# Optimization experiments

Hardware: AMD Instinct MI355X
Metric: run time of the kernel (lower is better)

## Reference

```python
import jax, jax.numpy as jnp
import numpy as np

B = 8
WS = 7; NH = 8; HD = 16; C = 128; HP = 56; SHIFT = 3; L = HP * HP
SCALE = HD ** -0.5


def _rel_pos_index():
    coords = np.stack(np.meshgrid(np.arange(WS), np.arange(WS), indexing='ij')).reshape(2, -1)
    rel = (coords[:, :, None] - coords[:, None, :]).transpose(1, 2, 0)
    rel[:, :, 0] += WS - 1
    rel[:, :, 1] += WS - 1
    rel[:, :, 0] *= 2 * WS - 1
    return rel.sum(-1)  # (49, 49) int


def _attn_mask():
    img = np.zeros((HP, HP))
    cnt = 0
    for h in (slice(0, -WS), slice(-WS, -SHIFT), slice(-SHIFT, None)):
        for w in (slice(0, -WS), slice(-WS, -SHIFT), slice(-SHIFT, None)):
            img[h, w] = cnt
            cnt += 1
    m = img.reshape(HP // WS, WS, HP // WS, WS).transpose(0, 2, 1, 3).reshape(-1, WS * WS)
    am = m[:, None, :] - m[:, :, None]
    return np.where(am != 0, -100.0, 0.0).astype(np.float32)  # (64, 49, 49)


REL_IDX = _rel_pos_index()
ATTN_MASK = jnp.asarray(_attn_mask())


def _ln(x, g, b):
    mu = x.mean(-1, keepdims=True)
    v = ((x - mu) ** 2).mean(-1, keepdims=True)
    return (x - mu) / jnp.sqrt(v + 1e-5) * g + b


def setup_inputs() -> dict:
    key = jax.random.key(0)
    ks = iter(jax.random.split(key, 40))
    n = lambda shape: jax.random.normal(next(ks), shape, dtype=jnp.float32) * 0.02
    z = lambda shape: jnp.zeros(shape, dtype=jnp.float32)
    o = lambda shape: jnp.ones(shape, dtype=jnp.float32)
    return dict(
        infrared=jax.random.normal(next(ks), (B, 1, 224, 224), dtype=jnp.float32),
        visible=jax.random.normal(next(ks), (B, 1, 224, 224), dtype=jnp.float32),
        patch_w=n((16, C)), patch_b=z((C,)),
        pn_g=o((C,)), pn_b=z((C,)),
        pos_embed=n((1, L, C)),
        norm1_g=o((2, C)), norm1_b=z((2, C)),
        qkv_w=n((2, C, 3 * C)), qkv_b=z((2, 3 * C)),
        proj_w=n((2, C, C)), proj_b=z((2, C)),
        norm2_g=o((2, C)), norm2_b=z((2, C)),
        fc1_w=n((2, C, 4 * C)), fc1_b=z((2, 4 * C)),
        fc2_w=n((2, 4 * C, C)), fc2_b=z((2, C)),
        rpb=n((2, (2 * WS - 1) ** 2, NH)),
        normf_g=o((C,)), normf_b=z((C,)),
        head1_w=n((C, 256)), head1_b=z((256,)),
        head2_w=n((256, 1)), head2_b=z((1,)),
    )


def reference(infrared, visible, patch_w, patch_b, pn_g, pn_b, pos_embed,
              norm1_g, norm1_b, qkv_w, qkv_b, proj_w, proj_b,
              norm2_g, norm2_b, fc1_w, fc1_b, fc2_w, fc2_b, rpb,
              normf_g, normf_b, head1_w, head1_b, head2_w, head2_b):
    Bv = visible.shape[0]
    # 4x4 stride-4 conv on 1-channel input == patchify + matmul
    x = visible.reshape(Bv, HP, 4, HP, 4).transpose(0, 1, 3, 2, 4).reshape(Bv, L, 16)
    x = _ln(x @ patch_w + patch_b, pn_g, pn_b) + pos_embed  # (B, 3136, 128)

    def win_attn(xw, i, mask):
        Bn, N = xw.shape[0], WS * WS
        qkv = (xw @ qkv_w[i] + qkv_b[i]).reshape(Bn, N, 3, NH, HD).transpose(2, 0, 3, 1, 4)
        q, k, v = qkv[0], qkv[1], qkv[2]
        attn = jnp.einsum('bhnd,bhmd->bhnm', q * SCALE, k)  # (Bn, H, 49, 49)
        bias = rpb[i][REL_IDX.reshape(-1)].reshape(N, N, NH).transpose(2, 0, 1)
        attn = attn + bias[None]
        if mask is not None:
            attn = attn.reshape(Bv, -1, NH, N, N) + mask[None, :, None]
            attn = attn.reshape(Bn, NH, N, N)
        attn = jax.nn.softmax(attn, axis=-1)
        out = jnp.einsum('bhnm,bhmd->bhnd', attn, v).transpose(0, 2, 1, 3).reshape(Bn, N, C)
        return out @ proj_w[i] + proj_b[i]

    def block(x, i, shift):
        shortcut = x
        h = _ln(x, norm1_g[i], norm1_b[i]).reshape(Bv, HP, HP, C)
        if shift:
            h = jnp.roll(h, (-SHIFT, -SHIFT), (1, 2))
        w = h.reshape(Bv, 8, WS, 8, WS, C).transpose(0, 1, 3, 2, 4, 5).reshape(-1, WS * WS, C)
        w = win_attn(w, i, ATTN_MASK if shift else None)
        h = w.reshape(Bv, 8, 8, WS, WS, C).transpose(0, 1, 3, 2, 4, 5).reshape(Bv, HP, HP, C)
        if shift:
            h = jnp.roll(h, (SHIFT, SHIFT), (1, 2))
        x = shortcut + h.reshape(Bv, L, C)  # drop_path is identity at inference
        m = _ln(x, norm2_g[i], norm2_b[i])
        m = jax.nn.gelu(m @ fc1_w[i] + fc1_b[i]) @ fc2_w[i] + fc2_b[i]
        return x + m

    x = block(x, 0, False)
    x = block(x, 1, True)
    x = jax.nn.relu(_ln(x, normf_g, normf_b))          # (B, 3136, 128)
    x = x.reshape(Bv, C, HP, HP)                       # raw view, as in torch code
    x = jnp.repeat(jnp.repeat(x, 4, axis=2), 4, axis=3)  # nearest 56 -> 224
    x = x.reshape(Bv, 224 * 224, C)                    # raw view
    x = jax.nn.relu(x @ head1_w + head1_b) @ head2_w + head2_b
    return x.reshape(Bv, 1, 224, 224)
```

## Files before the change

### kernel.cpp

```cpp
#include <hip/hip_runtime.h>
#include <math.h>

#define DEV __device__ __forceinline__

constexpr int B_   = 8;
constexpr int NTOK = 25088;
constexpr int WGc  = 512;
constexpr int N2c  = 49;
constexpr int HDc  = 16;
constexpr int NHc  = 8;
constexpr float SCALEq = 0.25f;

typedef _Float16 f16x8 __attribute__((ext_vector_type(8)));
typedef float    f32x4 __attribute__((ext_vector_type(4)));

DEV float wave_sum(float v) {
#pragma unroll
  for (int m = 32; m >= 1; m >>= 1) v += __shfl_xor(v, m);
  return v;
}

DEV float gelu_f(float x) {
  float y = 0.7978845608028654f * (x + 0.044715f * x * x * x);
  return x / (1.f + __expf(-2.f * y));
}

DEV int win_map(int row, int shift) {
  int wg = row / 49, n = row - wg * 49;
  int b = wg >> 6, win = wg & 63;
  int sh = ((win >> 3) * 7) + n / 7;
  int sw = ((win & 7) * 7) + (n % 7);
  sh += shift; if (sh >= 56) sh -= 56;
  sw += shift; if (sw >= 56) sw -= 56;
  return b * 3136 + sh * 56 + sw;
}

DEV void split8(const float* __restrict__ x, ushort* hp, ushort* lp) {
  f16x8 h, l;
#pragma unroll
  for (int j = 0; j < 8; ++j) {
    float v = x[j];
    _Float16 hh = (_Float16)v;
    h[j] = hh;
    l[j] = (_Float16)(v - (float)hh);
  }
  *(f16x8*)hp = h;
  *(f16x8*)lp = l;
}

__global__ __launch_bounds__(128)
void patch_k(const float* __restrict__ vis, const float* __restrict__ pw,
             const float* __restrict__ pb, const float* __restrict__ g,
             const float* __restrict__ bb, const float* __restrict__ pos,
             float* __restrict__ X) {
  int row = blockIdx.x;
  int c = threadIdx.x;
  int b = row / 3136, l = row - b * 3136;
  int hp = l / 56, wp = l - hp * 56;
  __shared__ float p[16];
  __shared__ float red[2];
  if (c < 16) {
    int r = c >> 2, cc = c & 3;
    p[c] = vis[(long)b * 50176 + (hp * 4 + r) * 224 + wp * 4 + cc];
  }
  __syncthreads();
  float t = pb[c];
#pragma unroll
  for (int k = 0; k < 16; ++k) t = fmaf(p[k], pw[k * 128 + c], t);
  float s = wave_sum(t);
  if ((c & 63) == 0) red[c >> 6] = s;
  __syncthreads();
  float mu = (red[0] + red[1]) * (1.f / 128.f);
  __syncthreads();
  float d = t - mu;
  float s2 = wave_sum(d * d);
  if ((c & 63) == 0) red[c >> 6] = s2;
  __syncthreads();
  float var = (red[0] + red[1]) * (1.f / 128.f);
  float o = d * rsqrtf(var + 1e-5f) * g[c] + bb[c] + pos[(long)l * 128 + c];
  X[(long)row * 128 + c] = o;
}

__global__ __launch_bounds__(256)
void ln_k(const float* __restrict__ Xi, float* __restrict__ Out,
          const float* __restrict__ g, const float* __restrict__ b, int do_relu) {
  int row = blockIdx.x * 4 + (threadIdx.x >> 6);
  int lane = threadIdx.x & 63;
  long base = (long)row * 128 + lane * 2;
  float2 v = *(const float2*)&Xi[base];
  float mu = wave_sum(v.x + v.y) * (1.f / 128.f);
  float dx = v.x - mu, dy = v.y - mu;
  float var = wave_sum(dx * dx + dy * dy) * (1.f / 128.f);
  float r = rsqrtf(var + 1e-5f);
  float2 gg = *(const float2*)&g[lane * 2];
  float2 bb = *(const float2*)&b[lane * 2];
  float ox = dx * r * gg.x + bb.x;
  float oy = dy * r * gg.y + bb.y;
  if (do_relu) { ox = fmaxf(ox, 0.f); oy = fmaxf(oy, 0.f); }
  *(float2*)&Out[base] = make_float2(ox, oy);
}

template<int OUT_MODE, int ACT, int GATHER_A>
__global__ __launch_bounds__(256)
void mgemm_k(const float* __restrict__ A, const float* __restrict__ W,
             const float* __restrict__ bias, float* __restrict__ Out,
             int N, int K, int lda, int shift) {
  __shared__ __align__(16) ushort Ah[2048], Al[2048];
  __shared__ __align__(16) ushort Bh[4096], Bl[4096];
  int tid = threadIdx.x;
  int m0 = blockIdx.x * 64, n0 = blockIdx.y * 128;
  int lane = tid & 63, wid = tid >> 6;
  int wm = wid >> 1, wn = wid & 1;

  f32x4 acc[2][4];
#pragma unroll
  for (int mi = 0; mi < 2; ++mi)
#pragma unroll
    for (int ni = 0; ni < 4; ++ni) acc[mi][ni] = (f32x4){0.f, 0.f, 0.f, 0.f};

  int sr = tid >> 2;
  int sk8 = tid & 3;
  long asrc = GATHER_A ? (long)win_map(m0 + sr, shift) * lda
                       : (long)(m0 + sr) * lda;
  int achunk = ((sr >> 4) * 64 + sk8 * 16 + (sr & 15)) * 8;

  int bn0_ = tid & 127, bk80 = tid >> 7;
  int bn1_ = bn0_, bk81 = bk80 + 2;
  int bchunk0 = ((bn0_ >> 4) * 64 + bk80 * 16 + (bn0_ & 15)) * 8;
  int bchunk1 = ((bn1_ >> 4) * 64 + bk81 * 16 + (bn1_ & 15)) * 8;

  float areg[8], breg0[8], breg1[8];
  auto loadA = [&](int k0) {
    float4 t0 = *(const float4*)&A[asrc + k0 + sk8 * 8];
    float4 t1 = *(const float4*)&A[asrc + k0 + sk8 * 8 + 4];
    areg[0] = t0.x; areg[1] = t0.y; areg[2] = t0.z; areg[3] = t0.w;
    areg[4] = t1.x; areg[5] = t1.y; areg[6] = t1.z; areg[7] = t1.w;
  };
  auto loadB = [&](int k0) {
#pragma unroll
    for (int j = 0; j < 8; ++j)
      breg0[j] = W[(long)(k0 + bk80 * 8 + j) * N + n0 + bn0_];
#pragma unroll
    for (int j = 0; j < 8; ++j)
      breg1[j] = W[(long)(k0 + bk81 * 8 + j) * N + n0 + bn1_];
  };

  loadA(0); loadB(0);
  for (int k0 = 0; k0 < K; k0 += 32) {
    __syncthreads();
    split8(areg, &Ah[achunk], &Al[achunk]);
    split8(breg0, &Bh[bchunk0], &Bl[bchunk0]);
    split8(breg1, &Bh[bchunk1], &Bl[bchunk1]);
    __syncthreads();
    if (k0 + 32 < K) { loadA(k0 + 32); loadB(k0 + 32); }

    f16x8 ah[2], al[2], bh[4], bl[4];
#pragma unroll
    for (int mi = 0; mi < 2; ++mi) {
      int c = ((wm * 2 + mi) * 64 + lane) * 8;
      ah[mi] = *(const f16x8*)&Ah[c];
      al[mi] = *(const f16x8*)&Al[c];
    }
#pragma unroll
    for (int ni = 0; ni < 4; ++ni) {
      int c = ((wn * 4 + ni) * 64 + lane) * 8;
      bh[ni] = *(const f16x8*)&Bh[c];
      bl[ni] = *(const f16x8*)&Bl[c];
    }
#pragma unroll
    for (int mi = 0; mi < 2; ++mi)
#pragma unroll
      for (int ni = 0; ni < 4; ++ni) {
        acc[mi][ni] = __builtin_amdgcn_mfma_f32_16x16x32_f16(ah[mi], bh[ni], acc[mi][ni], 0, 0, 0);
        acc[mi][ni] = __builtin_amdgcn_mfma_f32_16x16x32_f16(ah[mi], bl[ni], acc[mi][ni], 0, 0, 0);
        acc[mi][ni] = __builtin_amdgcn_mfma_f32_16x16x32_f16(al[mi], bh[ni], acc[mi][ni], 0, 0, 0);
      }
  }

  int r4 = (lane >> 4) * 4, cb = lane & 15;
#pragma unroll
  for (int mi = 0; mi < 2; ++mi) {
#pragma unroll
    for (int rr = 0; rr < 4; ++rr) {
      int row = m0 + wm * 32 + mi * 16 + r4 + rr;
      int dst = (OUT_MODE == 2) ? win_map(row, shift) : row;
#pragma unroll
      for (int ni = 0; ni < 4; ++ni) {
        int col = n0 + wn * 64 + ni * 16 + cb;
        float val = acc[mi][ni][rr] + bias[col];
        if (ACT == 1) val = gelu_f(val);
        if (OUT_MODE == 0) {
          Out[(long)row * N + col] = val;
        } else if (OUT_MODE == 1) {
          int t = col >> 7, cc = col & 127, h = cc >> 4, d = cc & 15;
          if (t == 0) val *= SCALEq;
          int wg = row / 49, n = row - wg * 49;
          Out[((((long)t * WGc + wg) * NHc + h) * N2c + n) * HDc + d] = val;
        } else {
          Out[(long)dst * 128 + col] += val;
        }
      }
    }
  }
}

__global__ __launch_bounds__(256)
void attn_k(const float* __restrict__ QKV, float* __restrict__ AO,
            const float* __restrict__ rpb, int shift) {
  int wg = blockIdx.x >> 3;
  int h  = blockIdx.x & 7;
  int tid = threadIdx.x;
  __shared__ float Qs[49][17], Ks[49][17], Vs[49][17];
  __shared__ float S[49][50];
  const float* Qp = QKV + (((long)0 * WGc + wg) * NHc + h) * N2c * HDc;
  const float* Kp = QKV + (((long)1 * WGc + wg) * NHc + h) * N2c * HDc;
  const float* Vp = QKV + (((long)2 * WGc + wg) * NHc + h) * N2c * HDc;
  for (int idx = tid; idx < 49 * 16; idx += 256) {
    int n = idx >> 4, d = idx & 15;
    Qs[n][d] = Qp[idx]; Ks[n][d] = Kp[idx]; Vs[n][d] = Vp[idx];
  }
  __syncthreads();
  int win = wg & 63, wy = win >> 3, wx = win & 7;
  for (int idx = tid; idx < 49 * 49; idx += 256) {
    int i = idx / 49, j = idx - i * 49;
    float s = 0.f;
#pragma unroll
    for (int d = 0; d < 16; ++d) s = fmaf(Qs[i][d], Ks[j][d], s);
    int pyi = i / 7, pxi = i - pyi * 7, pyj = j / 7, pxj = j - pyj * 7;
    int rel = (pyi - pyj + 6) * 13 + (pxi - pxj + 6);
    s += rpb[rel * 8 + h];
    if (shift) {
      int shi = wy * 7 + pyi, swi = wx * 7 + pxi;
      int shj = wy * 7 + pyj, swj = wx * 7 + pxj;
      int ri = (shi < 49 ? 0 : (shi < 53 ? 1 : 2)) * 3 + (swi < 49 ? 0 : (swi < 53 ? 1 : 2));
      int rj = (shj < 49 ? 0 : (shj < 53 ? 1 : 2)) * 3 + (swj < 49 ? 0 : (swj < 53 ? 1 : 2));
      if (ri != rj) s -= 100.f;
    }
    S[i][j] = s;
  }
  __syncthreads();
  int lane = tid & 63, wv = tid >> 6;
  for (int i = wv; i < 49; i += 4) {
    float v = lane < 49 ? S[i][lane] : -1e30f;
    float m = v;
#pragma unroll
    for (int d = 32; d >= 1; d >>= 1) m = fmaxf(m, __shfl_xor(m, d));
    float e = lane < 49 ? __expf(v - m) : 0.f;
    float s = e;
#pragma unroll
    for (int d = 32; d >= 1; d >>= 1) s += __shfl_xor(s, d);
    if (lane < 49) S[i][lane] = e / s;
  }
  __syncthreads();
  for (int idx = tid; idx < 49 * 16; idx += 256) {
    int i = idx >> 4, d = idx & 15;
    float o = 0.f;
    for (int j = 0; j < 49; ++j) o = fmaf(S[i][j], Vs[j][d], o);
    AO[((long)wg * 49 + i) * 128 + h * 16 + d] = o;
  }
}

__global__ __launch_bounds__(256)
void w1split_k(const float* __restrict__ W1, ushort* __restrict__ Bh_g,
               ushort* __restrict__ Bl_g) {
  int a = blockIdx.x, c = threadIdx.x;
  float s = W1[(4 * a + 0) * 256 + c] + W1[(4 * a + 1) * 256 + c] +
            W1[(4 * a + 2) * 256 + c] + W1[(4 * a + 3) * 256 + c];
  _Float16 h = (_Float16)s;
  _Float16 l = (_Float16)(s - (float)h);
  int idx = ((c >> 4) * 64 + (a >> 3) * 16 + (c & 15)) * 8 + (a & 7);
  Bh_g[idx] = *(const ushort*)&h;
  Bl_g[idx] = *(const ushort*)&l;
}

__global__ __launch_bounds__(256)
void head_mfma_k(const float* __restrict__ Y, const ushort* __restrict__ Bh_g,
                 const ushort* __restrict__ Bl_g, const float* __restrict__ b1,
                 const float* __restrict__ W2, const float* __restrict__ b2,
                 float* __restrict__ Out) {
  __shared__ __align__(16) ushort Ah[2048], Al[2048];
  __shared__ __align__(16) ushort Bh[8192], Bl[8192];
  int tid = threadIdx.x;
  int m0 = blockIdx.x * 64;
  int lane = tid & 63, w = tid >> 6;

  {
    int sr = tid >> 2, sk8 = tid & 3;
    int rg = m0 + sr;
    int b = rg / 50176;
    int r = rg - b * 50176;
    int ch = r / 392;
    int s = r - ch * 392;
    long ybase = (long)b * 401408 + (long)ch * 3136;
    float av[8];
#pragma unroll
    for (int j = 0; j < 8; ++j) {
      int t = s * 128 + (sk8 * 8 + j) * 4;
      int H = t / 224, Wp = t - H * 224;
      av[j] = Y[ybase + (H >> 2) * 56 + (Wp >> 2)];
    }
    int chunk = ((sr >> 4) * 64 + sk8 * 16 + (sr & 15)) * 8;
    split8(av, &Ah[chunk], &Al[chunk]);
  }
  for (int i = tid; i < 1024; i += 256) {
    *(f16x8*)&Bh[i * 8] = *(const f16x8*)&Bh_g[i * 8];
    *(f16x8*)&Bl[i * 8] = *(const f16x8*)&Bl_g[i * 8];
  }
  float b1v[16], w2v[16];
#pragma unroll
  for (int ni = 0; ni < 16; ++ni) {
    b1v[ni] = b1[ni * 16 + (lane & 15)];
    w2v[ni] = W2[ni * 16 + (lane & 15)];
  }
  __syncthreads();

  f16x8 ah = *(const f16x8*)&Ah[(w * 64 + lane) * 8];
  f16x8 al = *(const f16x8*)&Al[(w * 64 + lane) * 8];
  float p[4] = {0.f, 0.f, 0.f, 0.f};
#pragma unroll
  for (int ni = 0; ni < 16; ++ni) {
    f16x8 bh = *(const f16x8*)&Bh[(ni * 64 + lane) * 8];
    f16x8 bl = *(const f16x8*)&Bl[(ni * 64 + lane) * 8];
    f32x4 acc = (f32x4){0.f, 0.f, 0.f, 0.f};
    acc = __builtin_amdgcn_mfma_f32_16x16x32_f16(ah, bh, acc, 0, 0, 0);
    acc = __builtin_amdgcn_mfma_f32_16x16x32_f16(ah, bl, acc, 0, 0, 0);
    acc = __builtin_amdgcn_mfma_f32_16x16x32_f16(al, bh, acc, 0, 0, 0);
#pragma unroll
    for (int reg = 0; reg < 4; ++reg) {
      float hval = fmaxf(acc[reg] + b1v[ni], 0.f);
      p[reg] = fmaf(hval, w2v[ni], p[reg]);
    }
  }
  float b2v = b2[0];
#pragma unroll
  for (int reg = 0; reg < 4; ++reg) {
#pragma unroll
    for (int d = 1; d < 16; d <<= 1) p[reg] += __shfl_xor(p[reg], d);
    if ((lane & 15) == 0)
      Out[m0 + w * 16 + (lane >> 4) * 4 + reg] = p[reg] + b2v;
  }
}

extern "C" void kernel_launch(void* const* d_in, const int* in_sizes, int n_in,
                              void* d_out, int out_size, void* d_ws, size_t ws_size,
                              hipStream_t stream) {
  const float* visible = (const float*)d_in[1];
  const float* patch_w = (const float*)d_in[2];
  const float* patch_b = (const float*)d_in[3];
  const float* pn_g    = (const float*)d_in[4];
  const float* pn_b    = (const float*)d_in[5];
  const float* pos     = (const float*)d_in[6];
  const float* norm1_g = (const float*)d_in[7];
  const float* norm1_b = (const float*)d_in[8];
  const float* qkv_w   = (const float*)d_in[9];
  const float* qkv_b   = (const float*)d_in[10];
  const float* proj_w  = (const float*)d_in[11];
  const float* proj_b  = (const float*)d_in[12];
  const float* norm2_g = (const float*)d_in[13];
  const float* norm2_b = (const float*)d_in[14];
  const float* fc1_w   = (const float*)d_in[15];
  const float* fc1_b   = (const float*)d_in[16];
  const float* fc2_w   = (const float*)d_in[17];
  const float* fc2_b   = (const float*)d_in[18];
  const float* rpb     = (const float*)d_in[19];
  const float* normf_g = (const float*)d_in[20];
  const float* normf_b = (const float*)d_in[21];
  const float* h1w     = (const float*)d_in[22];
  const float* h1b     = (const float*)d_in[23];
  const float* h2w     = (const float*)d_in[24];
  const float* h2b     = (const float*)d_in[25];
  float* out = (float*)d_out;

  float* X   = (float*)d_ws;
  float* XN  = X  + (long)NTOK * 128;
  float* BIG = XN + (long)NTOK * 128;
  float* QKV = BIG;
  float* AO  = BIG + (long)NTOK * 384;
  float* Hb  = BIG;
  float* Y   = XN;
  ushort* BHG = (ushort*)BIG;
  ushort* BLG = BHG + 8192;

  patch_k<<<NTOK, 128, 0, stream>>>(visible, patch_w, patch_b, pn_g, pn_b, pos, X);

  for (int layer = 0; layer < 2; ++layer) {
    int shift = layer ? 3 : 0;
    ln_k<<<NTOK / 4, 256, 0, stream>>>(X, XN, norm1_g + layer * 128, norm1_b + layer * 128, 0);
    mgemm_k<1, 0, 1><<<dim3(392, 3), 256, 0, stream>>>(
        XN, qkv_w + (long)layer * 128 * 384, qkv_b + layer * 384, QKV, 384, 128, 128, shift);
    attn_k<<<WGc * 8, 256, 0, stream>>>(QKV, AO, rpb + (long)layer * 169 * 8, shift);
    mgemm_k<2, 0, 0><<<dim3(392, 1), 256, 0, stream>>>(
        AO, proj_w + (long)layer * 128 * 128, proj_b + layer * 128, X, 128, 128, 128, shift);
    ln_k<<<NTOK / 4, 256, 0, stream>>>(X, XN, norm2_g + layer * 128, norm2_b + layer * 128, 0);
    mgemm_k<0, 1, 0><<<dim3(392, 4), 256, 0, stream>>>(
        XN, fc1_w + (long)layer * 128 * 512, fc1_b + layer * 512, Hb, 512, 128, 128, 0);
    mgemm_k<3, 0, 0><<<dim3(392, 1), 256, 0, stream>>>(
        Hb, fc2_w + (long)layer * 512 * 128, fc2_b + layer * 128, X, 128, 512, 512, 0);
  }

  ln_k<<<NTOK / 4, 256, 0, stream>>>(X, Y, normf_g, normf_b, 1);
  w1split_k<<<32, 256, 0, stream>>>(h1w, BHG, BLG);
  head_mfma_k<<<6272, 256, 0, stream>>>(Y, BHG, BLG, h1b, h2w, h2b, out);
}
```

Measured before the change: 485.4 us.

## Rewrite window attention with fp16 MFMA and precomputed relative-position bias table

Replaces the scalar per-(window,head) attention kernel with an MFMA-based kernel where each block handles one window and each wave processes two heads, computing QK^T and PV with 16x16x32 fp16 MFMA and doing the softmax in registers via 16-lane shuffles. A new small kernel expands the relative position bias into a dense per-head 49x49 table stored in the XN buffer, which is free at that point. Probabilities are staged in swizzled LDS for the PV product. This cuts scalar FMA and LDS traffic but lowers Q, K, V and P to fp16, which reduces precision, and it adds an extra kernel launch per layer.

```diff
diff --git a/kernel.cpp b/kernel.cpp
--- a/kernel.cpp
+++ b/kernel.cpp
@@ -205,58 +205,154 @@
 }
 
 __global__ __launch_bounds__(256)
-void attn_k(const float* __restrict__ QKV, float* __restrict__ AO,
-            const float* __restrict__ rpb, int shift) {
-  int wg = blockIdx.x >> 3;
-  int h  = blockIdx.x & 7;
+void bias_k(const float* __restrict__ rpb, float* __restrict__ tbl) {
+  int idx = blockIdx.x * 256 + threadIdx.x;
+  if (idx >= 8 * 2401) return;
+  int h = idx / 2401, r = idx - h * 2401;
+  int i = r / 49, j = r - i * 49;
+  int pyi = i / 7, pxi = i - pyi * 7, pyj = j / 7, pxj = j - pyj * 7;
+  int rel = (pyi - pyj + 6) * 13 + (pxi - pxj + 6);
+  tbl[idx] = rpb[rel * 8 + h];
+}
+
+__global__ __launch_bounds__(256)
+void attn_mfma_k(const float* __restrict__ QKV, float* __restrict__ AO,
+                 const float* __restrict__ btbl, int shift) {
+  __shared__ __align__(16) _Float16 Pl[4][64][64];
   int tid = threadIdx.x;
-  __shared__ float Qs[49][17], Ks[49][17], Vs[49][17];
-  __shared__ float S[49][50];
-  const float* Qp = QKV + (((long)0 * WGc + wg) * NHc + h) * N2c * HDc;
-  const float* Kp = QKV + (((long)1 * WGc + wg) * NHc + h) * N2c * HDc;
-  const float* Vp = QKV + (((long)2 * WGc + wg) * NHc + h) * N2c * HDc;
-  for (int idx = tid; idx < 49 * 16; idx += 256) {
-    int n = idx >> 4, d = idx & 15;
-    Qs[n][d] = Qp[idx]; Ks[n][d] = Kp[idx]; Vs[n][d] = Vp[idx];
-  }
-  __syncthreads();
+  int wg = blockIdx.x;
+  int lane = tid & 63, w = tid >> 6;
+  int li = lane & 15, lk = lane >> 4;
   int win = wg & 63, wy = win >> 3, wx = win & 7;
-  for (int idx = tid; idx < 49 * 49; idx += 256) {
-    int i = idx / 49, j = idx - i * 49;
-    float s = 0.f;
-#pragma unroll
-    for (int d = 0; d < 16; ++d) s = fmaf(Qs[i][d], Ks[j][d], s);
-    int pyi = i / 7, pxi = i - pyi * 7, pyj = j / 7, pxj = j - pyj * 7;
-    int rel = (pyi - pyj + 6) * 13 + (pxi - pxj + 6);
-    s += rpb[rel * 8 + h];
-    if (shift) {
-      int shi = wy * 7 + pyi, swi = wx * 7 + pxi;
-      int shj = wy * 7 + pyj, swj = wx * 7 + pxj;
-      int ri = (shi < 49 ? 0 : (shi < 53 ? 1 : 2)) * 3 + (swi < 49 ? 0 : (swi < 53 ? 1 : 2));
-      int rj = (shj < 49 ? 0 : (shj < 53 ? 1 : 2)) * 3 + (swj < 49 ? 0 : (swj < 53 ? 1 : 2));
-      if (ri != rj) s -= 100.f;
-    }
-    S[i][j] = s;
-  }
-  __syncthreads();
-  int lane = tid & 63, wv = tid >> 6;
-  for (int i = wv; i < 49; i += 4) {
-    float v = lane < 49 ? S[i][lane] : -1e30f;
-    float m = v;
-#pragma unroll
-    for (int d = 32; d >= 1; d >>= 1) m = fmaxf(m, __shfl_xor(m, d));
-    float e = lane < 49 ? __expf(v - m) : 0.f;
-    float s = e;
-#pragma unroll
-    for (int d = 32; d >= 1; d >>= 1) s += __shfl_xor(s, d);
-    if (lane < 49) S[i][lane] = e / s;
-  }
-  __syncthreads();
-  for (int idx = tid; idx < 49 * 16; idx += 256) {
-    int i = idx >> 4, d = idx & 15;
-    float o = 0.f;
-    for (int j = 0; j < 49; ++j) o = fmaf(S[i][j], Vs[j][d], o);
-    AO[((long)wg * 49 + i) * 128 + h * 16 + d] = o;
+
+  int ri[4][4], rj[4];
+  if (shift) {
+#pragma unroll
+    for (int mi = 0; mi < 4; ++mi)
+#pragma unroll
+      for (int reg = 0; reg < 4; ++reg) {
+        int i = mi * 16 + lk * 4 + reg;
+        int py = i / 7, px = i - py * 7;
+        int sh = wy * 7 + py, sw = wx * 7 + px;
+        ri[mi][reg] = (sh < 49 ? 0 : (sh < 53 ? 1 : 2)) * 3 + (sw < 49 ? 0 : (sw < 53 ? 1 : 2));
+      }
+#pragma unroll
+    for (int nj = 0; nj < 4; ++nj) {
+      int j = nj * 16 + li;
+      int py = j / 7, px = j - py * 7;
+      int sh = wy * 7 + py, sw = wx * 7 + px;
+      rj[nj] = (sh < 49 ? 0 : (sh < 53 ? 1 : 2)) * 3 + (sw < 49 ? 0 : (sw < 53 ? 1 : 2));
+    }
+  }
+
+  for (int hh = 0; hh < 2; ++hh) {
+    int h = w * 2 + hh;
+    const float* Qp = QKV + (((long)0 * WGc + wg) * NHc + h) * 784;
+    const float* Kp = QKV + (((long)1 * WGc + wg) * NHc + h) * 784;
+    const float* Vp = QKV + (((long)2 * WGc + wg) * NHc + h) * 784;
+
+    f16x8 qf[4], kf[4];
+#pragma unroll
+    for (int t = 0; t < 4; ++t) {
+      f16x8 q, k;
+#pragma unroll
+      for (int e = 0; e < 8; ++e) { q[e] = (_Float16)0.f; k[e] = (_Float16)0.f; }
+      int r = t * 16 + li;
+      if (lk < 2 && r < 49) {
+        const float* pq = &Qp[r * 16 + lk * 8];
+        const float* pk = &Kp[r * 16 + lk * 8];
+#pragma unroll
+        for (int e = 0; e < 8; ++e) {
+          q[e] = (_Float16)pq[e];
+          k[e] = (_Float16)pk[e];
+        }
+      }
+      qf[t] = q; kf[t] = k;
+    }
+
+    f32x4 s[4][4];
+#pragma unroll
+    for (int mi = 0; mi < 4; ++mi)
+#pragma unroll
+      for (int nj = 0; nj < 4; ++nj) {
+        f32x4 z = (f32x4){0.f, 0.f, 0.f, 0.f};
+        s[mi][nj] = __builtin_amdgcn_mfma_f32_16x16x32_f16(qf[mi], kf[nj], z, 0, 0, 0);
+      }
+
+    const float* bth = btbl + (long)h * 2401;
+    char* pbase = (char*)&Pl[w][0][0];
+#pragma unroll
+    for (int mi = 0; mi < 4; ++mi) {
+#pragma unroll
+      for (int reg = 0; reg < 4; ++reg) {
+        int i = mi * 16 + lk * 4 + reg;
+        float sv[4];
+#pragma unroll
+        for (int nj = 0; nj < 4; ++nj) {
+          int j = nj * 16 + li;
+          float v = -1e30f;
+          if (i < 49 && j < 49) {
+            v = s[mi][nj][reg] + bth[i * 49 + j];
+            if (shift && ri[mi][reg] != rj[nj]) v -= 100.f;
+          }
+          sv[nj] = v;
+        }
+        float m = fmaxf(fmaxf(sv[0], sv[1]), fmaxf(sv[2], sv[3]));
+#pragma unroll
+        for (int d = 1; d < 16; d <<= 1) m = fmaxf(m, __shfl_xor(m, d));
+        float e0 = __expf(sv[0] - m), e1 = __expf(sv[1] - m);
+        float e2 = __expf(sv[2] - m), e3 = __expf(sv[3] - m);
+        float sum = e0 + e1 + e2 + e3;
+#pragma unroll
+        for (int d = 1; d < 16; d <<= 1) sum += __shfl_xor(sum, d);
+        float inv = 1.f / sum;
+        int rL = i;
+        int sw4 = (rL & 7) << 4;
+        float ee[4] = {e0, e1, e2, e3};
+#pragma unroll
+        for (int nj = 0; nj < 4; ++nj) {
+          int byte = rL * 128 + (((nj * 16 + li) * 2) ^ sw4);
+          *(_Float16*)(pbase + byte) = (_Float16)(ee[nj] * inv);
+        }
+      }
+    }
+    __syncthreads();
+
+    f16x8 vf[2];
+#pragma unroll
+    for (int ks = 0; ks < 2; ++ks) {
+      f16x8 v;
+#pragma unroll
+      for (int e = 0; e < 8; ++e) {
+        int j = ks * 32 + lk * 8 + e;
+        v[e] = (j < 49) ? (_Float16)Vp[j * 16 + li] : (_Float16)0.f;
+      }
+      vf[ks] = v;
+    }
+
+    f32x4 o[4];
+#pragma unroll
+    for (int mi = 0; mi < 4; ++mi) {
+      f32x4 acc = (f32x4){0.f, 0.f, 0.f, 0.f};
+#pragma unroll
+      for (int ks = 0; ks < 2; ++ks) {
+        int row = mi * 16 + li;
+        int byte = row * 128 + (((ks * 32 + lk * 8) * 2) ^ ((row & 7) << 4));
+        f16x8 pf = *(const f16x8*)(pbase + byte);
+        acc = __builtin_amdgcn_mfma_f32_16x16x32_f16(pf, vf[ks], acc, 0, 0, 0);
+      }
+      o[mi] = acc;
+    }
+#pragma unroll
+    for (int mi = 0; mi < 4; ++mi) {
+#pragma unroll
+      for (int reg = 0; reg < 4; ++reg) {
+        int i = mi * 16 + lk * 4 + reg;
+        if (i < 49)
+          AO[((long)wg * 49 + i) * 128 + h * 16 + li] = o[mi][reg];
+      }
+    }
+    __syncthreads();
   }
 }
 
@@ -378,6 +474,7 @@
   float* AO  = BIG + (long)NTOK * 384;
   float* Hb  = BIG;
   float* Y   = XN;
+  float* BT  = XN;
   ushort* BHG = (ushort*)BIG;
   ushort* BLG = BHG + 8192;
 
@@ -388,7 +485,8 @@
     ln_k<<<NTOK / 4, 256, 0, stream>>>(X, XN, norm1_g + layer * 128, norm1_b + layer * 128, 0);
     mgemm_k<1, 0, 1><<<dim3(392, 3), 256, 0, stream>>>(
         XN, qkv_w + (long)layer * 128 * 384, qkv_b + layer * 384, QKV, 384, 128, 128, shift);
-    attn_k<<<WGc * 8, 256, 0, stream>>>(QKV, AO, rpb + (long)layer * 169 * 8, shift);
+    bias_k<<<76, 256, 0, stream>>>(rpb + (long)layer * 169 * 8, BT);
+    attn_mfma_k<<<WGc, 256, 0, stream>>>(QKV, AO, BT, shift);
     mgemm_k<2, 0, 0><<<dim3(392, 1), 256, 0, stream>>>(
         AO, proj_w + (long)layer * 128 * 128, proj_b + layer * 128, X, 128, 128, 128, shift);
     ln_k<<<NTOK / 4, 256, 0, stream>>>(X, XN, norm2_g + layer * 128, norm2_b + layer * 128, 0);
```

Measured after the change: 462.7 us. 1.05x faster.
